# Optimization experiments

Measured on AMD Instinct MI355X. Metric: run time of the kernel, lower is better.

The kernel has to match this reference:

```python
import jax, jax.numpy as jnp
import numpy as np

TAU = 0.5

def setup_inputs() -> dict:
    key = jax.random.key(0)
    ks = jax.random.split(key, 20)
    B, D1, D2, E1, E2, U = 4096, 2000, 2000, 256, 256, 512
    M = E1 + E2
    s = lambda k, shp, scale=0.05: jax.random.normal(k, shp, dtype=jnp.float32) * scale
    return {
        "inputs": jax.random.normal(ks[0], (B, D1 + D2), dtype=jnp.float32),
        "h_tm1": jax.random.normal(ks[1], (B, U), dtype=jnp.float32),
        "crohis_tm": jax.random.normal(ks[2], (B, M), dtype=jnp.float32),
        "embed_weight_1": s(ks[3], (D1, E1)),
        "embed_weight_2": s(ks[4], (D2, E2)),
        "ca_1to2_w": s(ks[5], (E1, E1)),
        "ca_1to2_u": s(ks[6], (E2, E1)),
        "ca_1to2_v": s(ks[7], (E2, E1)),
        "ca_2to1_w": s(ks[8], (E2, E2)),
        "ca_2to1_u": s(ks[9], (E1, E2)),
        "ca_2to1_v": s(ks[10], (E1, E2)),
        "crohis_weight_w": s(ks[11], (M, U)),
        "crohis_bias": jnp.zeros((U,), jnp.float32),
        "crohis_decomp_weight": s(ks[12], (M, M)),
        "crohis_decomp_bias": jnp.zeros((M,), jnp.float32),
        "kernel": s(ks[13], (M, 3 * U)),
        "recurrent_kernel": s(ks[14], (U, 3 * U)),
        "bias": jnp.zeros((3 * U,), jnp.float32),
    }


def reference(inputs, h_tm1, crohis_tm,
              embed_weight_1, embed_weight_2,
              ca_1to2_w, ca_1to2_u, ca_1to2_v,
              ca_2to1_w, ca_2to1_u, ca_2to1_v,
              crohis_weight_w, crohis_bias,
              crohis_decomp_weight, crohis_decomp_bias,
              kernel, recurrent_kernel, bias):
    D1 = embed_weight_1.shape[0]
    U = recurrent_kernel.shape[0]
    # dual embedding lookups (dense multi-hot x embedding matrix)
    seqx1 = inputs[:, :D1]
    seqx2 = inputs[:, D1:]
    emb1 = seqx1 @ embed_weight_1   # [B, E1]
    emb2 = seqx2 @ embed_weight_2   # [B, E2]
    # cross-attention gates (softmax over feature axis, as K.softmax default)
    att12 = jax.nn.softmax(jnp.tanh(emb1 @ ca_1to2_w + emb2 @ ca_1to2_u) * (emb2 @ ca_1to2_v), axis=-1)
    att21 = jax.nn.softmax(jnp.tanh(emb2 @ ca_2to1_w + emb1 @ ca_2to1_u) * (emb1 @ ca_2to1_v), axis=-1)
    x = jnp.concatenate([emb1 * att12, emb2 * att21], axis=-1)  # [B, M]
    # cross-history decomposition modulating previous hidden state
    cro = jnp.tanh(crohis_tm @ crohis_decomp_weight + crohis_decomp_bias)
    h_prev = h_tm1 + jnp.tanh(cro @ crohis_weight_w + crohis_bias)
    # GRU (implementation=2, reset_after=False)
    mx = x @ kernel + bias                         # [B, 3U]
    x_z, x_r, x_h = mx[:, :U], mx[:, U:2 * U], mx[:, 2 * U:]
    mi = h_prev @ recurrent_kernel[:, :2 * U]      # [B, 2U]
    z = jax.nn.sigmoid(x_z + mi[:, :U])
    r = jax.nn.sigmoid(x_r + mi[:, U:])
    hh = jnp.tanh(x_h + (r * h_prev) @ recurrent_kernel[:, 2 * U:])
    h = z * h_prev + (1.0 - z) * hh
    # updated cross-history state (exponential moving average with tau)
    crohis_new = TAU * crohis_tm + (1.0 - TAU) * x
    return h, crohis_new
```

## Files before the change

kernel.cpp:

```cpp
#include <hip/hip_runtime.h>
#include <hip/hip_bf16.h>
#include <math.h>


#define TAU_F 0.5f

typedef __bf16 bf16x8 __attribute__((ext_vector_type(8)));
typedef __bf16 bf16x4 __attribute__((ext_vector_type(4)));
typedef float f32x4 __attribute__((ext_vector_type(4)));

__device__ __forceinline__ void gload16(const void* g, void* l) {
    __builtin_amdgcn_global_load_lds(
        (const __attribute__((address_space(1))) void*)g,
        (__attribute__((address_space(3))) void*)l, 16, 0, 0);
}

struct SubGemm {
    const void* A;
    int lda;
    int Kvalid;
    const __bf16* BT;
    int ldbt;
    float* C;
    int ldc;
    long long strideC;
    int Ksub;
    int nbx;
    int pairSplit;
    int pairAOff;
};

template <bool AFP32>
__global__ __launch_bounds__(256) void gemm_dual(SubGemm g1, SubGemm g2, int blocks1)
{
    __shared__ __bf16 As[2][64][32];
    __shared__ __bf16 Bs[2][128][32];

    const int tid = threadIdx.x, w = tid >> 6, l = tid & 63;
    const bool second = (int)blockIdx.x >= blocks1;
    const SubGemm& g = second ? g2 : g1;
    const int bxl = second ? (int)blockIdx.x - blocks1 : (int)blockIdx.x;
    const int ct = bxl % g.nbx, spl = bxl / g.nbx;
    const int brow = (int)blockIdx.y * 64, bcol = ct * 128;
    const int k_begin = spl * g.Ksub;
    const int nt = g.Ksub >> 5;
    float* C = g.C + (size_t)spl * g.strideC;
    const int aoff = (ct >= g.pairSplit) ? g.pairAOff : 0;

    const int sar = w * 16 + (l >> 2);
    const int sbr = w * 32 + (l >> 2);
    const int seg = (l & 3) * 8;

    const __bf16* Ab = (const __bf16*)g.A + aoff + (size_t)(brow + sar) * g.lda + seg + k_begin;
    const float*  Af = (const float*)g.A + aoff + (size_t)(brow + sar) * g.lda + seg + k_begin;
    const __bf16* Bg0 = g.BT + (size_t)(bcol + sbr) * g.ldbt + seg + k_begin;
    const __bf16* Bg1 = Bg0 + (size_t)16 * g.ldbt;

    f32x4 acc[2][4] = {};
    const int fr = l & 15, fk = (l >> 4) * 8;
    const int wr = (w >> 1) * 32, wc = (w & 1) * 64;

    if (AFP32) {
        int c0 = k_begin + seg;
        f32x4 v0 = {0,0,0,0}, v1 = {0,0,0,0};
        if (c0     < g.Kvalid) v0 = *(const f32x4*)(Af);
        if (c0 + 4 < g.Kvalid) v1 = *(const f32x4*)(Af + 4);
        gload16(Bg0, &Bs[0][w * 32][0]);
        gload16(Bg1, &Bs[0][w * 32 + 16][0]);
        asm volatile("s_waitcnt vmcnt(0)" ::: "memory");
        __bf16 o[8];
#pragma unroll
        for (int q = 0; q < 4; ++q) { o[q] = (__bf16)v0[q]; o[4 + q] = (__bf16)v1[q]; }
        *(bf16x8*)&As[0][sar][seg] = *(bf16x8*)o;
    } else {
        gload16(Ab, &As[0][w * 16][0]);
        gload16(Bg0, &Bs[0][w * 32][0]);
        gload16(Bg1, &Bs[0][w * 32 + 16][0]);
    }
    __syncthreads();

    int cur = 0;
    for (int t = 0; t < nt; ++t) {
        bf16x8 a[2], b[4];
#pragma unroll
        for (int m = 0; m < 2; ++m) a[m] = *(const bf16x8*)&As[cur][wr + m * 16 + fr][fk];
#pragma unroll
        for (int n = 0; n < 4; ++n) b[n] = *(const bf16x8*)&Bs[cur][wc + n * 16 + fr][fk];

        f32x4 v0 = {0,0,0,0}, v1 = {0,0,0,0};
        const bool more = (t + 1 < nt);
        if (more) {
            const int k = (t + 1) * 32;
            if (AFP32) {
                int c0 = k_begin + seg + k;
                if (c0     < g.Kvalid) v0 = *(const f32x4*)(Af + k);
                if (c0 + 4 < g.Kvalid) v1 = *(const f32x4*)(Af + k + 4);
            } else {
                gload16(Ab + k, &As[cur ^ 1][w * 16][0]);
            }
            gload16(Bg0 + k, &Bs[cur ^ 1][w * 32][0]);
            gload16(Bg1 + k, &Bs[cur ^ 1][w * 32 + 16][0]);
        }

#pragma unroll
        for (int m = 0; m < 2; ++m)
#pragma unroll
            for (int n = 0; n < 4; ++n)
                acc[m][n] = __builtin_amdgcn_mfma_f32_16x16x32_bf16(a[m], b[n], acc[m][n], 0, 0, 0);

        if (AFP32 && more) {
            asm volatile("s_waitcnt vmcnt(0)" ::: "memory");
            __bf16 o[8];
#pragma unroll
            for (int q = 0; q < 4; ++q) { o[q] = (__bf16)v0[q]; o[4 + q] = (__bf16)v1[q]; }
            *(bf16x8*)&As[cur ^ 1][sar][seg] = *(bf16x8*)o;
        }
        __syncthreads();
        cur ^= 1;
    }

    const int fq = (l >> 4) * 4;
#pragma unroll
    for (int m = 0; m < 2; ++m)
#pragma unroll
        for (int n = 0; n < 4; ++n)
#pragma unroll
            for (int r = 0; r < 4; ++r) {
                int row = brow + wr + m * 16 + fq + r;
                int col = bcol + wc + n * 16 + fr;
                C[(size_t)row * g.ldc + col] = acc[m][n][r];
            }
}

__global__ __launch_bounds__(256) void prep_w(
    const float* __restrict__ ew1, const float* __restrict__ ew2,
    const float* __restrict__ w12, const float* __restrict__ u12,
    const float* __restrict__ v12, const float* __restrict__ w21,
    const float* __restrict__ u21, const float* __restrict__ v21,
    const float* __restrict__ cd_w, const float* __restrict__ cw_w,
    const float* __restrict__ kern, const float* __restrict__ rkern,
    __bf16* __restrict__ WT, __bf16* __restrict__ WcatT,
    __bf16* __restrict__ cdT, __bf16* __restrict__ cwT,
    __bf16* __restrict__ kernT, __bf16* __restrict__ rkernT)
{
    int idx = blockIdx.x * 256 + threadIdx.x;
    if (idx < 1048576) {
        int n = idx >> 11, k = idx & 2047;
        float v = 0.f;
        if (k < 2000) v = (n < 256) ? ew1[(size_t)k * 256 + n]
                                    : ew2[(size_t)k * 256 + (n - 256)];
        WT[idx] = (__bf16)v;
        return;
    }
    idx -= 1048576;
    if (idx < 524288) {
        int n = idx >> 9, k = idx & 511;
        int jm = n & 255; bool khi = k >= 256; int kk = k & 255;
        float v;
        if (n < 256)      v = khi ? u12[kk * 256 + jm] : w12[kk * 256 + jm];
        else if (n < 512) v = khi ? w21[kk * 256 + jm] : u21[kk * 256 + jm];
        else if (n < 768) v = khi ? v12[kk * 256 + jm] : 0.f;
        else              v = khi ? 0.f : v21[kk * 256 + jm];
        WcatT[idx] = (__bf16)v;
        return;
    }
    idx -= 524288;
    if (idx < 262144) {
        int n = idx >> 9, k = idx & 511;
        cdT[idx] = (__bf16)cd_w[(size_t)k * 512 + n];
        return;
    }
    idx -= 262144;
    if (idx < 262144) {
        int n = idx >> 9, k = idx & 511;
        cwT[idx] = (__bf16)cw_w[(size_t)k * 512 + n];
        return;
    }
    idx -= 262144;
    if (idx < 786432) {
        int n = idx >> 9, k = idx & 511;
        kernT[idx] = (__bf16)kern[(size_t)k * 1536 + n];
        return;
    }
    idx -= 786432;
    if (idx < 786432) {
        int n = idx >> 9, k = idx & 511;
        rkernT[idx] = (__bf16)rkern[(size_t)k * 1536 + n];
    }
}

__global__ __launch_bounds__(256) void reduce_A(
    const float* __restrict__ P12, const float* __restrict__ P4,
    const float* __restrict__ cd_b,
    __bf16* __restrict__ E, __bf16* __restrict__ cro)
{
    int b = blockIdx.x;
    int i = (((b & 2047) * 256) + threadIdx.x) * 4;
    if (b < 2048) {
        f32x4 p0 = *(const f32x4*)(P12 + i);
        f32x4 p1 = *(const f32x4*)(P12 + (1 << 21) + i);
        __bf16 o[4];
#pragma unroll
        for (int j = 0; j < 4; ++j) o[j] = (__bf16)(p0[j] + p1[j]);
        *(bf16x4*)&E[i] = *(bf16x4*)o;
    } else {
        f32x4 p0 = *(const f32x4*)(P4 + i);
        int c = i & 511;
        __bf16 o[4];
#pragma unroll
        for (int j = 0; j < 4; ++j) o[j] = (__bf16)tanhf(p0[j] + cd_b[c + j]);
        *(bf16x4*)&cro[i] = *(bf16x4*)o;
    }
}

__global__ __launch_bounds__(256) void fuse1(
    const float* __restrict__ T, const __bf16* __restrict__ E,
    const float* __restrict__ crohis,
    const float* __restrict__ P5,
    const float* __restrict__ h_tm1, const float* __restrict__ cw_b,
    __bf16* __restrict__ x, float* __restrict__ cro_out,
    float* __restrict__ hprev, __bf16* __restrict__ hprev_bf)
{
    __shared__ float s4[4];
    int b = blockIdx.x;
    int j = threadIdx.x;
    if (b < 4096) {
        const float* t = T + (size_t)b * 1024;
        float s12 = tanhf(t[j])       * t[512 + j];
        float s21 = tanhf(t[256 + j]) * t[768 + j];
        float v = s12;
#pragma unroll
        for (int o = 32; o >= 1; o >>= 1) v = fmaxf(v, __shfl_xor(v, o, 64));
        __syncthreads(); if ((j & 63) == 0) s4[j >> 6] = v; __syncthreads();
        float m12 = fmaxf(fmaxf(s4[0], s4[1]), fmaxf(s4[2], s4[3]));
        float e12 = expf(s12 - m12);
        v = e12;
#pragma unroll
        for (int o = 32; o >= 1; o >>= 1) v += __shfl_xor(v, o, 64);
        __syncthreads(); if ((j & 63) == 0) s4[j >> 6] = v; __syncthreads();
        float sum12 = s4[0] + s4[1] + s4[2] + s4[3];
        v = s21;
#pragma unroll
        for (int o = 32; o >= 1; o >>= 1) v = fmaxf(v, __shfl_xor(v, o, 64));
        __syncthreads(); if ((j & 63) == 0) s4[j >> 6] = v; __syncthreads();
        float m21 = fmaxf(fmaxf(s4[0], s4[1]), fmaxf(s4[2], s4[3]));
        float e21 = expf(s21 - m21);
        v = e21;
#pragma unroll
        for (int o = 32; o >= 1; o >>= 1) v += __shfl_xor(v, o, 64);
        __syncthreads(); if ((j & 63) == 0) s4[j >> 6] = v; __syncthreads();
        float sum21 = s4[0] + s4[1] + s4[2] + s4[3];

        size_t b0 = (size_t)b * 512 + j, b1 = b0 + 256;
        float x1 = (float)E[b0] * (e12 / sum12);
        float x2 = (float)E[b1] * (e21 / sum21);
        x[b0] = (__bf16)x1;
        x[b1] = (__bf16)x2;
        cro_out[b0] = TAU_F * crohis[b0] + (1.f - TAU_F) * x1;
        cro_out[b1] = TAU_F * crohis[b1] + (1.f - TAU_F) * x2;
    } else {
        int i = ((b - 4096) * 256 + j) * 4;
        f32x4 p = *(const f32x4*)(P5 + i);
        f32x4 ht = *(const f32x4*)(h_tm1 + i);
        int c = i & 511;
        f32x4 o; __bf16 ob[4];
#pragma unroll
        for (int q = 0; q < 4; ++q) {
            float hv = ht[q] + tanhf(p[q] + cw_b[c + q]);
            o[q] = hv; ob[q] = (__bf16)hv;
        }
        *(f32x4*)(hprev + i) = o;
        *(bf16x4*)&hprev_bf[i] = *(bf16x4*)ob;
    }
}

__global__ __launch_bounds__(256) void gates_k(
    const float* __restrict__ mx, const float* __restrict__ mi2,
    const float* __restrict__ hprev, const float* __restrict__ bias,
    __bf16* __restrict__ rh)
{
    int i = (blockIdx.x * 256 + threadIdx.x) * 4;
    int row = i >> 9, c = i & 511;
    f32x4 a  = *(const f32x4*)(mx + (size_t)row * 1536 + 512 + c);
    f32x4 m  = *(const f32x4*)(mi2 + (size_t)row * 1024 + 512 + c);
    f32x4 hp = *(const f32x4*)(hprev + i);
    f32x4 bb = *(const f32x4*)(bias + 512 + c);
    __bf16 o[4];
#pragma unroll
    for (int q = 0; q < 4; ++q) {
        float r = 1.f / (1.f + expf(-(a[q] + bb[q] + m[q])));
        o[q] = (__bf16)(r * hp[q]);
    }
    *(bf16x4*)&rh[i] = *(bf16x4*)o;
}

__global__ __launch_bounds__(256) void final_k(
    const float* __restrict__ mx, const float* __restrict__ mi2,
    const float* __restrict__ P8a, const float* __restrict__ P8b,
    const float* __restrict__ hprev, const float* __restrict__ bias,
    float* __restrict__ h)
{
    int i = (blockIdx.x * 256 + threadIdx.x) * 4;
    int row = i >> 9, c = i & 511;
    f32x4 xz = *(const f32x4*)(mx + (size_t)row * 1536 + c);
    f32x4 xh = *(const f32x4*)(mx + (size_t)row * 1536 + 1024 + c);
    f32x4 mz = *(const f32x4*)(mi2 + (size_t)row * 1024 + c);
    f32x4 p0 = *(const f32x4*)(P8a + i);
    f32x4 p1 = *(const f32x4*)(P8b + i);
    f32x4 hp = *(const f32x4*)(hprev + i);
    f32x4 bz = *(const f32x4*)(bias + c);
    f32x4 bh = *(const f32x4*)(bias + 1024 + c);
    f32x4 o;
#pragma unroll
    for (int q = 0; q < 4; ++q) {
        float z = 1.f / (1.f + expf(-(xz[q] + bz[q] + mz[q])));
        float hh = tanhf(xh[q] + bh[q] + p0[q] + p1[q]);
        o[q] = z * hp[q] + (1.f - z) * hh;
    }
    *(f32x4*)(h + i) = o;
}

extern "C" void kernel_launch(void* const* d_in, const int* in_sizes, int n_in,
                              void* d_out, int out_size, void* d_ws, size_t ws_size,
                              hipStream_t stream)
{
    (void)in_sizes; (void)n_in; (void)out_size; (void)ws_size;

    const float* inputs = (const float*)d_in[0];
    const float* h_tm1  = (const float*)d_in[1];
    const float* crohis = (const float*)d_in[2];
    const float* ew1    = (const float*)d_in[3];
    const float* ew2    = (const float*)d_in[4];
    const float* ca12w  = (const float*)d_in[5];
    const float* ca12u  = (const float*)d_in[6];
    const float* ca12v  = (const float*)d_in[7];
    const float* ca21w  = (const float*)d_in[8];
    const float* ca21u  = (const float*)d_in[9];
    const float* ca21v  = (const float*)d_in[10];
    const float* cw_w   = (const float*)d_in[11];
    const float* cw_b   = (const float*)d_in[12];
    const float* cd_w   = (const float*)d_in[13];
    const float* cd_b   = (const float*)d_in[14];
    const float* kern   = (const float*)d_in[15];
    const float* rkern  = (const float*)d_in[16];
    const float* bias   = (const float*)d_in[17];

    char* ws = (char*)d_ws;
    const size_t MB = 1 << 20;
    float*  P12      = (float*)(ws + 0);
    float*  P4       = (float*)(ws + 16 * MB);
    float*  T        = (float*)(ws + 0);
    float*  P5       = (float*)(ws + 16 * MB);
    float*  mx       = (float*)(ws + 0);
    float*  hprev    = (float*)(ws + 24 * MB);
    __bf16* E        = (__bf16*)(ws + 32 * MB);
    __bf16* rh       = (__bf16*)(ws + 32 * MB);
    __bf16* cro_bf   = (__bf16*)(ws + 36 * MB);
    __bf16* x        = (__bf16*)(ws + 36 * MB);
    __bf16* hprev_bf = (__bf16*)(ws + 40 * MB);
    float*  P8       = (float*)(ws + 36 * MB);
    float*  mi2      = (float*)(ws + 44 * MB);
    __bf16* WT       = (__bf16*)(ws + 68 * MB);
    __bf16* WcatT    = (__bf16*)(ws + 70 * MB);
    __bf16* cdT      = (__bf16*)(ws + 71 * MB);
    __bf16* cwT      = (__bf16*)(ws + 71 * MB + 512 * 1024);
    __bf16* kernT    = (__bf16*)(ws + 72 * MB);
    __bf16* rkernT   = (__bf16*)(ws + 73 * MB + 512 * 1024);

    float* h_out   = (float*)d_out;
    float* cro_out = (float*)d_out + 2 * 1048576;

    const int BIG = 1 << 30;

    prep_w<<<14336, 256, 0, stream>>>(ew1, ew2, ca12w, ca12u, ca12v, ca21w,
                                      ca21u, ca21v, cd_w, cw_w, kern, rkern,
                                      WT, WcatT, cdT, cwT, kernT, rkernT);

    SubGemm gA1 = { inputs, 4000, 2000, WT, 2048, P12, 512, 1ll << 21, 1024, 4, 2, 2000 };
    SubGemm gA2 = { crohis,  512,  512, cdT,  512, P4,  512, 0,         512, 4, BIG, 0 };
    gemm_dual<true><<<dim3(12, 64), 256, 0, stream>>>(gA1, gA2, 8);

    reduce_A<<<4096, 256, 0, stream>>>(P12, P4, cd_b, E, cro_bf);

    SubGemm gB1 = { E,      512, 512, WcatT, 512, T,  1024, 0, 512, 8, BIG, 0 };
    SubGemm gB2 = { cro_bf, 512, 512, cwT,   512, P5, 512,  0, 512, 4, BIG, 0 };
    gemm_dual<false><<<dim3(12, 64), 256, 0, stream>>>(gB1, gB2, 8);

    fuse1<<<6144, 256, 0, stream>>>(T, E, crohis, P5, h_tm1, cw_b,
                                    x, cro_out, hprev, hprev_bf);

    SubGemm gC1 = { x,        512, 512, kernT,  512, mx,  1536, 0, 512, 12, BIG, 0 };
    SubGemm gC2 = { hprev_bf, 512, 512, rkernT, 512, mi2, 1024, 0, 512, 8,  BIG, 0 };
    gemm_dual<false><<<dim3(20, 64), 256, 0, stream>>>(gC1, gC2, 12);

    gates_k<<<2048, 256, 0, stream>>>(mx, mi2, hprev, bias, rh);

    SubGemm gG = { rh, 512, 512, rkernT + (size_t)1024 * 512, 512, P8, 512, 6ll << 20, 256, 4, BIG, 0 };
    gemm_dual<false><<<dim3(8, 64), 256, 0, stream>>>(gG, gG, 8);

    final_k<<<2048, 256, 0, stream>>>(mx, mi2, P8, P8 + (6ll << 20), hprev, bias, h_out);
}
```

Measured before the change: 148.9 us.

## Triple-buffer GEMM K-loop with depth-2 prefetch and swizzled block mapping

The dual GEMM kernel moves from double to triple LDS buffering. Loads for tile t+2 are issued while tile t is computed, and partial vmcnt waits replace full drains and __syncthreads. It also remaps the linear workgroup id with a stride-8 swizzle, so neighbouring tiles share cache locality across dies, and it clamps out-of-range fp32 A columns instead of zero-masking them. This should hide more global-load latency, at the cost of extra LDS. It also depends on the grid size being divisible by 8 and on the padded B rows being zero, so the clamped A reads do not change results.

```diff
diff --git a/kernel.cpp b/kernel.cpp
--- a/kernel.cpp
+++ b/kernel.cpp
@@ -33,15 +33,23 @@
 template <bool AFP32>
 __global__ __launch_bounds__(256) void gemm_dual(SubGemm g1, SubGemm g2, int blocks1)
 {
-    __shared__ __bf16 As[2][64][32];
-    __shared__ __bf16 Bs[2][128][32];
+    __shared__ __bf16 As[3][64][32];
+    __shared__ __bf16 Bs[3][128][32];
 
     const int tid = threadIdx.x, w = tid >> 6, l = tid & 63;
-    const bool second = (int)blockIdx.x >= blocks1;
+
+    const int gx = gridDim.x;
+    const int nwg = gx * (int)gridDim.y;
+    const int hw = (int)blockIdx.y * gx + (int)blockIdx.x;
+    const int lg = (hw & 7) * (nwg >> 3) + (hw >> 3);
+    const int bxl_lin = lg % gx;
+    const int by = lg / gx;
+
+    const bool second = bxl_lin >= blocks1;
     const SubGemm& g = second ? g2 : g1;
-    const int bxl = second ? (int)blockIdx.x - blocks1 : (int)blockIdx.x;
+    const int bxl = second ? bxl_lin - blocks1 : bxl_lin;
     const int ct = bxl % g.nbx, spl = bxl / g.nbx;
-    const int brow = (int)blockIdx.y * 64, bcol = ct * 128;
+    const int brow = by * 64, bcol = ct * 128;
     const int k_begin = spl * g.Ksub;
     const int nt = g.Ksub >> 5;
     float* C = g.C + (size_t)spl * g.strideC;
@@ -51,55 +59,79 @@
     const int sbr = w * 32 + (l >> 2);
     const int seg = (l & 3) * 8;
 
-    const __bf16* Ab = (const __bf16*)g.A + aoff + (size_t)(brow + sar) * g.lda + seg + k_begin;
-    const float*  Af = (const float*)g.A + aoff + (size_t)(brow + sar) * g.lda + seg + k_begin;
+    const float*  AfRow = (const float*)g.A + aoff + (size_t)(brow + sar) * g.lda;
+    const __bf16* AbRow = (const __bf16*)g.A + aoff + (size_t)(brow + sar) * g.lda + seg + k_begin;
     const __bf16* Bg0 = g.BT + (size_t)(bcol + sbr) * g.ldbt + seg + k_begin;
     const __bf16* Bg1 = Bg0 + (size_t)16 * g.ldbt;
+    const int kcl = g.Kvalid - 8;
 
     f32x4 acc[2][4] = {};
     const int fr = l & 15, fk = (l >> 4) * 8;
     const int wr = (w >> 1) * 32, wc = (w & 1) * 64;
 
-    if (AFP32) {
-        int c0 = k_begin + seg;
-        f32x4 v0 = {0,0,0,0}, v1 = {0,0,0,0};
-        if (c0     < g.Kvalid) v0 = *(const f32x4*)(Af);
-        if (c0 + 4 < g.Kvalid) v1 = *(const f32x4*)(Af + 4);
+    f32x4 v0, v1;
+    if constexpr (AFP32) {
+        { int col = k_begin + seg; col = col < kcl ? col : kcl;
+          v0 = *(const f32x4*)(AfRow + col); v1 = *(const f32x4*)(AfRow + col + 4); }
         gload16(Bg0, &Bs[0][w * 32][0]);
         gload16(Bg1, &Bs[0][w * 32 + 16][0]);
-        asm volatile("s_waitcnt vmcnt(0)" ::: "memory");
-        __bf16 o[8];
-#pragma unroll
-        for (int q = 0; q < 4; ++q) { o[q] = (__bf16)v0[q]; o[4 + q] = (__bf16)v1[q]; }
-        *(bf16x8*)&As[0][sar][seg] = *(bf16x8*)o;
+        asm volatile("s_waitcnt vmcnt(2)" ::: "memory");
+        { __bf16 o[8];
+#pragma unroll
+          for (int z = 0; z < 4; ++z) { o[z] = (__bf16)v0[z]; o[4 + z] = (__bf16)v1[z]; }
+          *(bf16x8*)&As[0][sar][seg] = *(bf16x8*)o; }
+        { int col = k_begin + 32 + seg; col = col < kcl ? col : kcl;
+          v0 = *(const f32x4*)(AfRow + col); v1 = *(const f32x4*)(AfRow + col + 4); }
+        gload16(Bg0 + 32, &Bs[1][w * 32][0]);
+        gload16(Bg1 + 32, &Bs[1][w * 32 + 16][0]);
     } else {
-        gload16(Ab, &As[0][w * 16][0]);
-        gload16(Bg0, &Bs[0][w * 32][0]);
-        gload16(Bg1, &Bs[0][w * 32 + 16][0]);
-    }
-    __syncthreads();
-
-    int cur = 0;
+        gload16(AbRow,      &As[0][w * 16][0]);
+        gload16(Bg0,        &Bs[0][w * 32][0]);
+        gload16(Bg1,        &Bs[0][w * 32 + 16][0]);
+        gload16(AbRow + 32, &As[1][w * 16][0]);
+        gload16(Bg0 + 32,   &Bs[1][w * 32][0]);
+        gload16(Bg1 + 32,   &Bs[1][w * 32 + 16][0]);
+    }
+
+    int b0 = 0, b1 = 1, b2 = 2;
     for (int t = 0; t < nt; ++t) {
+        if (t < nt - 1) {
+            if constexpr (AFP32) asm volatile("s_waitcnt vmcnt(2)" ::: "memory");
+            else                 asm volatile("s_waitcnt vmcnt(3)" ::: "memory");
+        } else {
+            asm volatile("s_waitcnt vmcnt(0)" ::: "memory");
+        }
+        asm volatile("s_waitcnt lgkmcnt(0)" ::: "memory");
+        __builtin_amdgcn_s_barrier();
+
         bf16x8 a[2], b[4];
 #pragma unroll
-        for (int m = 0; m < 2; ++m) a[m] = *(const bf16x8*)&As[cur][wr + m * 16 + fr][fk];
-#pragma unroll
-        for (int n = 0; n < 4; ++n) b[n] = *(const bf16x8*)&Bs[cur][wc + n * 16 + fr][fk];
-
-        f32x4 v0 = {0,0,0,0}, v1 = {0,0,0,0};
-        const bool more = (t + 1 < nt);
-        if (more) {
-            const int k = (t + 1) * 32;
-            if (AFP32) {
-                int c0 = k_begin + seg + k;
-                if (c0     < g.Kvalid) v0 = *(const f32x4*)(Af + k);
-                if (c0 + 4 < g.Kvalid) v1 = *(const f32x4*)(Af + k + 4);
-            } else {
-                gload16(Ab + k, &As[cur ^ 1][w * 16][0]);
+        for (int m = 0; m < 2; ++m) a[m] = *(const bf16x8*)&As[b0][wr + m * 16 + fr][fk];
+#pragma unroll
+        for (int n = 0; n < 4; ++n) b[n] = *(const bf16x8*)&Bs[b0][wc + n * 16 + fr][fk];
+
+        if constexpr (AFP32) {
+            if (t + 1 < nt) {
+                __bf16 o[8];
+#pragma unroll
+                for (int z = 0; z < 4; ++z) { o[z] = (__bf16)v0[z]; o[4 + z] = (__bf16)v1[z]; }
+                *(bf16x8*)&As[b1][sar][seg] = *(bf16x8*)o;
             }
-            gload16(Bg0 + k, &Bs[cur ^ 1][w * 32][0]);
-            gload16(Bg1 + k, &Bs[cur ^ 1][w * 32 + 16][0]);
+            if (t + 2 < nt) {
+                const int k = (t + 2) * 32;
+                int col = k_begin + k + seg; col = col < kcl ? col : kcl;
+                v0 = *(const f32x4*)(AfRow + col);
+                v1 = *(const f32x4*)(AfRow + col + 4);
+                gload16(Bg0 + k, &Bs[b2][w * 32][0]);
+                gload16(Bg1 + k, &Bs[b2][w * 32 + 16][0]);
+            }
+        } else {
+            if (t + 2 < nt) {
+                const int k = (t + 2) * 32;
+                gload16(AbRow + k, &As[b2][w * 16][0]);
+                gload16(Bg0 + k,   &Bs[b2][w * 32][0]);
+                gload16(Bg1 + k,   &Bs[b2][w * 32 + 16][0]);
+            }
         }
 
 #pragma unroll
@@ -108,15 +140,7 @@
             for (int n = 0; n < 4; ++n)
                 acc[m][n] = __builtin_amdgcn_mfma_f32_16x16x32_bf16(a[m], b[n], acc[m][n], 0, 0, 0);
 
-        if (AFP32 && more) {
-            asm volatile("s_waitcnt vmcnt(0)" ::: "memory");
-            __bf16 o[8];
-#pragma unroll
-            for (int q = 0; q < 4; ++q) { o[q] = (__bf16)v0[q]; o[4 + q] = (__bf16)v1[q]; }
-            *(bf16x8*)&As[cur ^ 1][sar][seg] = *(bf16x8*)o;
-        }
-        __syncthreads();
-        cur ^= 1;
+        const int tmp = b0; b0 = b1; b1 = b2; b2 = tmp;
     }
 
     const int fq = (l >> 4) * 4;
```

Result: faster. 136.9 us (-8.0%).
